# Optimization experiments

Measured on AMD Instinct MI355X. Metric: run time of the kernel, lower is better.

The kernel has to match this reference:

```python
import jax, jax.numpy as jnp
import numpy as np

D_IN = 32
D_MODEL = 128
B, T = 512, 512
INPUT_DIM = 2 * D_IN  # concat_mask=True, d_u=0


def setup_inputs() -> dict:
    key = jax.random.key(0)
    ks = jax.random.split(key, 8)
    scale = 0.05
    return {
        "x": jax.random.normal(ks[0], (B, T, D_IN), dtype=jnp.float32),
        "W_ih": jax.random.normal(ks[1], (3 * D_MODEL, INPUT_DIM), dtype=jnp.float32) * scale,
        "W_hh": jax.random.normal(ks[2], (3 * D_MODEL, D_MODEL), dtype=jnp.float32) * scale,
        "b_ih": jax.random.normal(ks[3], (3 * D_MODEL,), dtype=jnp.float32) * scale,
        "b_hh": jax.random.normal(ks[4], (3 * D_MODEL,), dtype=jnp.float32) * scale,
        "W_out": jax.random.normal(ks[5], (D_IN, D_MODEL), dtype=jnp.float32) * scale,
        "b_out": jax.random.normal(ks[6], (D_IN,), dtype=jnp.float32) * scale,
        "mask": jax.random.randint(ks[7], (B, T, D_IN), 0, 2, dtype=jnp.int32),
    }


def reference(x, W_ih, W_hh, b_ih, b_hh, W_out, b_out, mask):
    m_bool = mask.astype(bool)                      # [B,T,d_in]
    m_f = mask.astype(x.dtype)
    x = jnp.where(m_bool, x, jnp.zeros_like(x))     # zero-fill missing

    h0 = jnp.zeros((x.shape[0], D_MODEL), dtype=x.dtype)   # state_init='zero'
    x_hat0 = h0 @ W_out.T + b_out                   # readout of initial state

    def gru_cell(x_t, h):
        gx = x_t @ W_ih.T + b_ih                    # [B, 3*d_model]
        gh = h @ W_hh.T + b_hh
        xr, xz, xn = jnp.split(gx, 3, axis=-1)
        hr, hz, hn = jnp.split(gh, 3, axis=-1)
        r = jax.nn.sigmoid(xr + hr)
        z = jax.nn.sigmoid(xz + hz)
        n = jnp.tanh(xn + r * hn)
        return (1.0 - z) * n + z * h

    def step(carry, inp):
        h, x_hat = carry
        x_s, mb_s, mf_s = inp                       # [B,d_in] each
        x_p = jnp.where(mb_s, x_s, x_hat)           # fill blanks with prediction
        x_t = jnp.concatenate([x_p, mf_s], axis=-1) # concat_mask=True
        h_new = gru_cell(x_t, h)
        x_hat_new = h_new @ W_out.T + b_out
        return (h_new, x_hat_new), x_hat_new

    # scan over steps 0..T-2 (time-major)
    xs = jnp.swapaxes(x[:, :-1], 0, 1)              # [T-1, B, d_in]
    mbs = jnp.swapaxes(m_bool[:, :-1], 0, 1)
    mfs = jnp.swapaxes(m_f[:, :-1], 0, 1)
    _, preds = jax.lax.scan(step, (h0, x_hat0), (xs, mbs, mfs))  # [T-1, B, d_in]

    out = jnp.concatenate([x_hat0[None], preds], axis=0)         # [T, B, d_in]
    return jnp.swapaxes(out, 0, 1)                                # [B, T, d_in]
```

## Files before the change

### kernel.cpp

```cpp
#include <hip/hip_runtime.h>
#include <hip/hip_bf16.h>

#define D_IN 32
#define TT 512
#define GB 16
#define NBLK 32
#define MAGIC 0x51F7C0DEu

typedef __attribute__((ext_vector_type(8))) short bf16x8;
typedef __attribute__((ext_vector_type(4))) float f32x4;
typedef __attribute__((ext_vector_type(4))) int   i32x4;

__device__ inline short bf16_of(float f) {
    union { float f; unsigned u; } v; v.f = f;
    unsigned r = v.u + 0x7FFFu + ((v.u >> 16) & 1u);
    return (short)(r >> 16);
}
__device__ inline unsigned cvt_pk_bf16(float lo, float hi) {
    unsigned r;
    asm("v_cvt_pk_bf16_f32 %0, %1, %2" : "=v"(r) : "v"(lo), "v"(hi));
    return r;
}
__device__ inline bf16x8 load8_bf16(const float* __restrict__ p) {
    bf16x8 r;
#pragma unroll
    for (int e = 0; e < 8; ++e) r[e] = bf16_of(p[e]);
    return r;
}
__device__ inline bf16x8 load44_bf16(const float* __restrict__ p, int qq) {
    bf16x8 r;
#pragma unroll
    for (int e = 0; e < 4; ++e) {
        r[e]     = bf16_of(p[qq * 4 + e]);
        r[4 + e] = bf16_of(p[16 + qq * 4 + e]);
    }
    return r;
}
__device__ inline f32x4 splat4(float v) { return (f32x4){v, v, v, v}; }

__device__ inline float sigmoid_fast(float x) {
    return __builtin_amdgcn_rcpf(1.0f + __expf(-x));
}
__device__ inline float tanh_fast(float x) {
    return 1.0f - 2.0f * __builtin_amdgcn_rcpf(__expf(2.0f * x) + 1.0f);
}
__device__ inline void lds_barrier() {
    asm volatile("s_waitcnt lgkmcnt(0)\n\ts_barrier" ::: "memory");
}

#define MFMA16(A, B, C) __builtin_amdgcn_mfma_f32_16x16x32_bf16(A, B, C, 0, 0, 0)

__global__ __launch_bounds__(512, 2)
void rnn_imputer(const float* __restrict__ x,
                 const float* __restrict__ W_ih,
                 const float* __restrict__ W_hh,
                 const float* __restrict__ b_ih,
                 const float* __restrict__ b_hh,
                 const float* __restrict__ W_out,
                 const float* __restrict__ b_out,
                 const int*   __restrict__ mask,
                 float* __restrict__ out,
                 unsigned*    flags,
                 int          use_spin) {
    if (blockIdx.x >= NBLK) {
        if (!use_spin || threadIdx.x >= 64) return;
        const unsigned long long t0 = __builtin_amdgcn_s_memrealtime();
        float a0 = 1.0f + threadIdx.x * 1e-6f, a1 = a0 + 0.1f, a2 = a0 + 0.2f,
              a3 = a0 + 0.3f, a4 = a0 + 0.4f, a5 = a0 + 0.5f, a6 = a0 + 0.6f,
              a7 = a0 + 0.7f;
        for (;;) {
            unsigned acc = 0;
#pragma unroll
            for (int j = 0; j < NBLK; ++j)
                acc |= (__hip_atomic_load(&flags[j], __ATOMIC_RELAXED,
                                          __HIP_MEMORY_SCOPE_AGENT) ^ MAGIC);
            if (acc == 0) break;
            if (__builtin_amdgcn_s_memrealtime() - t0 > 200000ull) break;
            for (int i = 0; i < 32; ++i) {
                a0 = __builtin_fmaf(a0, 1.0000001f, 1e-8f);
                a1 = __builtin_fmaf(a1, 1.0000001f, 1e-8f);
                a2 = __builtin_fmaf(a2, 1.0000001f, 1e-8f);
                a3 = __builtin_fmaf(a3, 1.0000001f, 1e-8f);
                a4 = __builtin_fmaf(a4, 1.0000001f, 1e-8f);
                a5 = __builtin_fmaf(a5, 1.0000001f, 1e-8f);
                a6 = __builtin_fmaf(a6, 1.0000001f, 1e-8f);
                a7 = __builtin_fmaf(a7, 1.0000001f, 1e-8f);
            }
            __builtin_amdgcn_s_sleep(8);
        }
        const float s = a0 + a1 + a2 + a3 + a4 + a5 + a6 + a7;
        if (s == 1.2345e30f) ((float*)flags)[NBLK + 1] = s;
        return;
    }

    __shared__ __align__(16) float xch[16][GB][36];
    __shared__ __align__(16) int   mch[16][GB][36];
    __shared__ __align__(16) short hbuf[2][GB][136];

    const int tid  = threadIdx.x;
    const int wv   = tid >> 6;
    const int lane = tid & 63;
    const int q    = lane >> 4;
    const int c    = lane & 15;
    const int bb   = blockIdx.x * GB;
    const int brow = bb + c;
    const int i_col = wv * 16 + c;

    bf16x8 Br[6], Bz[6], Bxn[2], Bhn[4];
    Br[0]  = load44_bf16(W_ih + (size_t)i_col * 64, q);
    Br[1]  = load44_bf16(W_ih + (size_t)i_col * 64 + 32, q);
    Bz[0]  = load44_bf16(W_ih + (size_t)(128 + i_col) * 64, q);
    Bz[1]  = load44_bf16(W_ih + (size_t)(128 + i_col) * 64 + 32, q);
    Bxn[0] = load44_bf16(W_ih + (size_t)(256 + i_col) * 64, q);
    Bxn[1] = load44_bf16(W_ih + (size_t)(256 + i_col) * 64 + 32, q);
#pragma unroll
    for (int kt = 2; kt < 6; ++kt) {
        const int k = (kt - 2) * 32 + q * 8;
        Br[kt] = load8_bf16(W_hh + (size_t)i_col * 128 + k);
        Bz[kt] = load8_bf16(W_hh + (size_t)(128 + i_col) * 128 + k);
    }
#pragma unroll
    for (int kt = 0; kt < 4; ++kt)
        Bhn[kt] = load8_bf16(W_hh + (size_t)(256 + i_col) * 128 + kt * 32 + q * 8);

    bf16x8 Ao[2][4];
#pragma unroll
    for (int ta = 0; ta < 2; ++ta)
#pragma unroll
        for (int kt = 0; kt < 4; ++kt)
            Ao[ta][kt] = load8_bf16(W_out + (size_t)(ta * 16 + c) * 128 + kt * 32 + q * 8);

    f32x4 bo_v[2];
#pragma unroll
    for (int ta = 0; ta < 2; ++ta)
        bo_v[ta] = *(const f32x4*)&b_out[ta * 16 + q * 4];

    const float bR  = b_ih[i_col]       + b_hh[i_col];
    const float bZ  = b_ih[128 + i_col] + b_hh[128 + i_col];
    const float bXN = b_ih[256 + i_col];
    const float bHN = b_hh[256 + i_col];

    float h_reg[4] = {0.f, 0.f, 0.f, 0.f};

    bf16x8 A0, A1;
    {
        const size_t o = (size_t)brow * TT * D_IN;
        const f32x4 xa = *(const f32x4*)&x[o + q * 4];
        const f32x4 xb = *(const f32x4*)&x[o + 16 + q * 4];
        const i32x4 ma = *(const i32x4*)&mask[o + q * 4];
        const i32x4 mb = *(const i32x4*)&mask[o + 16 + q * 4];
        union { bf16x8 v; unsigned d[4]; } a0, a1;
#pragma unroll
        for (int j = 0; j < 4; ++j) {
            const float fa = ma[j] ? xa[j] : b_out[q * 4 + j];
            const float fb = mb[j] ? xb[j] : b_out[16 + q * 4 + j];
            ((short*)&a0.v)[j]     = bf16_of(fa);
            ((short*)&a0.v)[4 + j] = bf16_of(fb);
            ((short*)&a1.v)[j]     = ma[j] ? (short)0x3F80 : (short)0;
            ((short*)&a1.v)[4 + j] = mb[j] ? (short)0x3F80 : (short)0;
        }
        A0 = a0.v; A1 = a1.v;
    }
#pragma unroll
    for (int ta = 0; ta < 2; ++ta)
        if (wv == ta)
            *(f32x4*)&out[(size_t)brow * TT * D_IN + ta * 16 + q * 4] = bo_v[ta];

#pragma unroll
    for (int rnd = 0; rnd < 4; ++rnd) {
        const int ts  = 1 + rnd * 4 + (tid >> 7);
        const int row = (tid >> 3) & 15;
        const int c4  = (tid & 7) * 4;
        const size_t o = ((size_t)(bb + row) * TT + ts) * D_IN + c4;
        *(f32x4*)&xch[ts & 15][row][c4] = *(const f32x4*)&x[o];
        *(i32x4*)&mch[ts & 15][row][c4] = *(const i32x4*)&mask[o];
    }

    f32x4 Ra = splat4(0.f), Rb = splat4(0.f);
    f32x4 Za = splat4(0.f), Zb = splat4(0.f);
    f32x4 HNa = splat4(bHN), HNb = splat4(0.f);
    f32x4 Rc  = MFMA16(A1, Br[1],  splat4(bR));
    f32x4 Zc  = MFMA16(A1, Bz[1],  splat4(bZ));
    f32x4 XNc = MFMA16(A1, Bxn[1], splat4(bXN));

    f32x4 sgx[2] = {splat4(0.f), splat4(0.f)};
    i32x4 sgm[2] = {(i32x4){0,0,0,0}, (i32x4){0,0,0,0}};

    __syncthreads();

    for (int t = 0; t < TT - 1; ++t) {
        Rc  = MFMA16(A0, Br[0],  Rc);
        Zc  = MFMA16(A0, Bz[0],  Zc);
        XNc = MFMA16(A0, Bxn[0], XNc);

        const int sl = (t + 1) & 15;
        const f32x4 pfx0 = *(const f32x4*)&xch[sl][c][q * 4];
        const f32x4 pfx1 = *(const f32x4*)&xch[sl][c][16 + q * 4];
        const i32x4 pfm0 = *(const i32x4*)&mch[sl][c][q * 4];
        const i32x4 pfm1 = *(const i32x4*)&mch[sl][c][16 + q * 4];

        {
            union { bf16x8 v; unsigned d[4]; } a1;
            a1.d[0] = (pfm0[0] ? 0x3F80u : 0u) | ((pfm0[1] ? 0x3F80u : 0u) << 16);
            a1.d[1] = (pfm0[2] ? 0x3F80u : 0u) | ((pfm0[3] ? 0x3F80u : 0u) << 16);
            a1.d[2] = (pfm1[0] ? 0x3F80u : 0u) | ((pfm1[1] ? 0x3F80u : 0u) << 16);
            a1.d[3] = (pfm1[2] ? 0x3F80u : 0u) | ((pfm1[3] ? 0x3F80u : 0u) << 16);
            A1 = a1.v;
        }
        f32x4 RcN  = MFMA16(A1, Br[1],  splat4(bR));
        f32x4 ZcN  = MFMA16(A1, Bz[1],  splat4(bZ));
        f32x4 XNcN = MFMA16(A1, Bxn[1], splat4(bXN));

        if ((t & 7) == 0 && t) {
#pragma unroll
            for (int rnd = 0; rnd < 2; ++rnd) {
                const int tsu = t + 8 + rnd * 4 + (tid >> 7);
                const int row = (tid >> 3) & 15;
                const int c4  = (tid & 7) * 4;
                *(f32x4*)&xch[tsu & 15][row][c4] = sgx[rnd];
                *(i32x4*)&mch[tsu & 15][row][c4] = sgm[rnd];
            }
        }
        if ((t & 7) == 7) {
#pragma unroll
            for (int rnd = 0; rnd < 2; ++rnd) {
                const int tsu = t + 9 + rnd * 4 + (tid >> 7);
                const int ts  = tsu <= TT - 1 ? tsu : TT - 1;
                const int row = (tid >> 3) & 15;
                const int c4  = (tid & 7) * 4;
                const size_t o = ((size_t)(bb + row) * TT + ts) * D_IN + c4;
                sgx[rnd] = *(const f32x4*)&x[o];
                sgm[rnd] = *(const i32x4*)&mask[o];
            }
        }

        const int pb = (t + 1) & 1;
        float hn[4];
#pragma unroll
        for (int r = 0; r < 4; ++r) {
            const float rr = sigmoid_fast(Ra[r] + Rb[r] + Rc[r]);
            const float zz = sigmoid_fast(Za[r] + Zb[r] + Zc[r]);
            const float nn = tanh_fast(XNc[r] + rr * (HNa[r] + HNb[r]));
            const float h  = nn + zz * (h_reg[r] - nn);
            h_reg[r] = h;
            hn[r] = h;
        }
        {
            const unsigned pk0 = cvt_pk_bf16(hn[0], hn[1]);
            const unsigned pk1 = cvt_pk_bf16(hn[2], hn[3]);
            hbuf[pb][q * 4 + 0][i_col] = (short)(pk0 & 0xFFFFu);
            hbuf[pb][q * 4 + 1][i_col] = (short)(pk0 >> 16);
            hbuf[pb][q * 4 + 2][i_col] = (short)(pk1 & 0xFFFFu);
            hbuf[pb][q * 4 + 3][i_col] = (short)(pk1 >> 16);
        }

        lds_barrier();

        bf16x8 Ah[4];
#pragma unroll
        for (int kt = 0; kt < 4; ++kt)
            Ah[kt] = *(const bf16x8*)&hbuf[pb][c][kt * 32 + q * 8];

        f32x4 o00 = MFMA16(Ao[0][0], Ah[0], bo_v[0]);
        f32x4 o10 = MFMA16(Ao[1][0], Ah[0], bo_v[1]);
        f32x4 o01 = MFMA16(Ao[0][1], Ah[1], splat4(0.f));
        f32x4 o11 = MFMA16(Ao[1][1], Ah[1], splat4(0.f));
        f32x4 o02 = MFMA16(Ao[0][2], Ah[2], splat4(0.f));
        f32x4 o12 = MFMA16(Ao[1][2], Ah[2], splat4(0.f));
        f32x4 o03 = MFMA16(Ao[0][3], Ah[3], splat4(0.f));
        f32x4 o13 = MFMA16(Ao[1][3], Ah[3], splat4(0.f));

        Ra  = MFMA16(Ah[0], Br[2], splat4(0.f));
        Za  = MFMA16(Ah[0], Bz[2], splat4(0.f));
        HNa = MFMA16(Ah[0], Bhn[0], splat4(bHN));
        Rb  = MFMA16(Ah[2], Br[4], splat4(0.f));
        Zb  = MFMA16(Ah[2], Bz[4], splat4(0.f));
        HNb = MFMA16(Ah[2], Bhn[2], splat4(0.f));
        Ra  = MFMA16(Ah[1], Br[3], Ra);
        Za  = MFMA16(Ah[1], Bz[3], Za);
        HNa = MFMA16(Ah[1], Bhn[1], HNa);
        Rb  = MFMA16(Ah[3], Br[5], Rb);
        Zb  = MFMA16(Ah[3], Bz[5], Zb);
        HNb = MFMA16(Ah[3], Bhn[3], HNb);

        {
            f32x4 xh0, xh1;
#pragma unroll
            for (int r = 0; r < 4; ++r) {
                xh0[r] = (o00[r] + o01[r]) + (o02[r] + o03[r]);
                xh1[r] = (o10[r] + o11[r]) + (o12[r] + o13[r]);
            }
            if (wv == 0)
                *(f32x4*)&out[((size_t)brow * TT + (t + 1)) * D_IN + q * 4] = xh0;
            if (wv == 1)
                *(f32x4*)&out[((size_t)brow * TT + (t + 1)) * D_IN + 16 + q * 4] = xh1;

            const float v00 = pfm0[0] ? pfx0[0] : xh0[0];
            const float v01 = pfm0[1] ? pfx0[1] : xh0[1];
            const float v02 = pfm0[2] ? pfx0[2] : xh0[2];
            const float v03 = pfm0[3] ? pfx0[3] : xh0[3];
            const float v10 = pfm1[0] ? pfx1[0] : xh1[0];
            const float v11 = pfm1[1] ? pfx1[1] : xh1[1];
            const float v12 = pfm1[2] ? pfx1[2] : xh1[2];
            const float v13 = pfm1[3] ? pfx1[3] : xh1[3];
            union { bf16x8 v; unsigned d[4]; } a0;
            a0.d[0] = cvt_pk_bf16(v00, v01);
            a0.d[1] = cvt_pk_bf16(v02, v03);
            a0.d[2] = cvt_pk_bf16(v10, v11);
            a0.d[3] = cvt_pk_bf16(v12, v13);
            A0 = a0.v;
        }

        Rc = RcN; Zc = ZcN; XNc = XNcN;
    }

    if (use_spin && tid == 0)
        __hip_atomic_store(&flags[blockIdx.x], MAGIC, __ATOMIC_RELAXED,
                           __HIP_MEMORY_SCOPE_AGENT);
}

extern "C" void kernel_launch(void* const* d_in, const int* in_sizes, int n_in,
                              void* d_out, int out_size, void* d_ws, size_t ws_size,
                              hipStream_t stream) {
    const float* x     = (const float*)d_in[0];
    const float* W_ih  = (const float*)d_in[1];
    const float* W_hh  = (const float*)d_in[2];
    const float* b_ih  = (const float*)d_in[3];
    const float* b_hh  = (const float*)d_in[4];
    const float* W_out = (const float*)d_in[5];
    const float* b_out = (const float*)d_in[6];
    const int*   mask  = (const int*)d_in[7];
    float* out = (float*)d_out;

    const int use_spin = (d_ws != nullptr && ws_size >= 256) ? 1 : 0;
    const int grid = use_spin ? 256 : NBLK;

    rnn_imputer<<<dim3(grid), dim3(512), 0, stream>>>(
        x, W_ih, W_hh, b_ih, b_hh, W_out, b_out, mask, out,
        (unsigned*)d_ws, use_spin);
}
```

Baseline: 664.6 us.

## Replace LDS x/mask staging with per-thread register prefetch and re-chain gate MFMAs

Removes the shared-memory ring buffer that staged x and mask in chunks of 8 steps. Each thread now loads its own row's x/mask for step t+2 directly from global memory into registers, one step ahead. The gate MFMA accumulation chains are reorganised so the mask-half of the input projection folds into the hidden accumulators, and the readout sums are chained pairwise. It also requests 72KB of dynamic shared memory, which likely limits how many blocks share a CU (the spin blocks). The trade is one global-load latency exposed per step against less LDS traffic and no periodic staging work.

```diff
diff --git a/kernel.cpp b/kernel.cpp
--- a/kernel.cpp
+++ b/kernel.cpp
@@ -49,6 +49,8 @@
 }
 
 #define MFMA16(A, B, C) __builtin_amdgcn_mfma_f32_16x16x32_bf16(A, B, C, 0, 0, 0)
+
+extern __shared__ char dyn_pad[];
 
 __global__ __launch_bounds__(512, 2)
 void rnn_imputer(const float* __restrict__ x,
@@ -93,8 +95,6 @@
         return;
     }
 
-    __shared__ __align__(16) float xch[16][GB][36];
-    __shared__ __align__(16) int   mch[16][GB][36];
     __shared__ __align__(16) short hbuf[2][GB][136];
 
     const int tid  = threadIdx.x;
@@ -142,13 +142,15 @@
 
     float h_reg[4] = {0.f, 0.f, 0.f, 0.f};
 
+    const float* xrow = x    + (size_t)brow * TT * D_IN + q * 4;
+    const int*   mrow = mask + (size_t)brow * TT * D_IN + q * 4;
+
     bf16x8 A0, A1;
     {
-        const size_t o = (size_t)brow * TT * D_IN;
-        const f32x4 xa = *(const f32x4*)&x[o + q * 4];
-        const f32x4 xb = *(const f32x4*)&x[o + 16 + q * 4];
-        const i32x4 ma = *(const i32x4*)&mask[o + q * 4];
-        const i32x4 mb = *(const i32x4*)&mask[o + 16 + q * 4];
+        const f32x4 xa = *(const f32x4*)&xrow[0];
+        const f32x4 xb = *(const f32x4*)&xrow[16];
+        const i32x4 ma = *(const i32x4*)&mrow[0];
+        const i32x4 mb = *(const i32x4*)&mrow[16];
         union { bf16x8 v; unsigned d[4]; } a0, a1;
 #pragma unroll
         for (int j = 0; j < 4; ++j) {
@@ -166,38 +168,82 @@
         if (wv == ta)
             *(f32x4*)&out[(size_t)brow * TT * D_IN + ta * 16 + q * 4] = bo_v[ta];
 
-#pragma unroll
-    for (int rnd = 0; rnd < 4; ++rnd) {
-        const int ts  = 1 + rnd * 4 + (tid >> 7);
-        const int row = (tid >> 3) & 15;
-        const int c4  = (tid & 7) * 4;
-        const size_t o = ((size_t)(bb + row) * TT + ts) * D_IN + c4;
-        *(f32x4*)&xch[ts & 15][row][c4] = *(const f32x4*)&x[o];
-        *(i32x4*)&mch[ts & 15][row][c4] = *(const i32x4*)&mask[o];
-    }
-
-    f32x4 Ra = splat4(0.f), Rb = splat4(0.f);
-    f32x4 Za = splat4(0.f), Zb = splat4(0.f);
+    f32x4 gx0 = *(const f32x4*)&xrow[1 * D_IN];
+    f32x4 gx1 = *(const f32x4*)&xrow[1 * D_IN + 16];
+    i32x4 gm0 = *(const i32x4*)&mrow[1 * D_IN];
+    i32x4 gm1 = *(const i32x4*)&mrow[1 * D_IN + 16];
+
+    f32x4 Ra = MFMA16(A1, Br[1],  splat4(bR));
+    f32x4 Za = MFMA16(A1, Bz[1],  splat4(bZ));
+    f32x4 XNa = MFMA16(A1, Bxn[1], splat4(bXN));
+    f32x4 Rb = splat4(0.f), Zb = splat4(0.f);
     f32x4 HNa = splat4(bHN), HNb = splat4(0.f);
-    f32x4 Rc  = MFMA16(A1, Br[1],  splat4(bR));
-    f32x4 Zc  = MFMA16(A1, Bz[1],  splat4(bZ));
-    f32x4 XNc = MFMA16(A1, Bxn[1], splat4(bXN));
-
-    f32x4 sgx[2] = {splat4(0.f), splat4(0.f)};
-    i32x4 sgm[2] = {(i32x4){0,0,0,0}, (i32x4){0,0,0,0}};
-
-    __syncthreads();
 
     for (int t = 0; t < TT - 1; ++t) {
-        Rc  = MFMA16(A0, Br[0],  Rc);
-        Zc  = MFMA16(A0, Bz[0],  Zc);
-        XNc = MFMA16(A0, Bxn[0], XNc);
-
-        const int sl = (t + 1) & 15;
-        const f32x4 pfx0 = *(const f32x4*)&xch[sl][c][q * 4];
-        const f32x4 pfx1 = *(const f32x4*)&xch[sl][c][16 + q * 4];
-        const i32x4 pfm0 = *(const i32x4*)&mch[sl][c][q * 4];
-        const i32x4 pfm1 = *(const i32x4*)&mch[sl][c][16 + q * 4];
+        Rb = MFMA16(A0, Br[0],  Rb);
+        Zb = MFMA16(A0, Bz[0],  Zb);
+        const f32x4 XNb = MFMA16(A0, Bxn[0], splat4(0.f));
+
+        const f32x4 pfx0 = gx0;
+        const f32x4 pfx1 = gx1;
+        const i32x4 pfm0 = gm0;
+        const i32x4 pfm1 = gm1;
+
+        const int ts2 = (t + 2 <= TT - 1) ? (t + 2) : (TT - 1);
+        const size_t o2 = (size_t)ts2 * D_IN;
+        const f32x4 nx0 = *(const f32x4*)&xrow[o2];
+        const f32x4 nx1 = *(const f32x4*)&xrow[o2 + 16];
+        const i32x4 nm0 = *(const i32x4*)&mrow[o2];
+        const i32x4 nm1 = *(const i32x4*)&mrow[o2 + 16];
+
+        const int pb = (t + 1) & 1;
+        float hn[4];
+#pragma unroll
+        for (int r = 0; r < 4; ++r) {
+            const float rr = sigmoid_fast(Ra[r] + Rb[r]);
+            const float zz = sigmoid_fast(Za[r] + Zb[r]);
+            const float nn = tanh_fast(XNa[r] + XNb[r] + rr * (HNa[r] + HNb[r]));
+            const float h  = nn + zz * (h_reg[r] - nn);
+            h_reg[r] = h;
+            hn[r] = h;
+        }
+        {
+            const unsigned pk0 = cvt_pk_bf16(hn[0], hn[1]);
+            const unsigned pk1 = cvt_pk_bf16(hn[2], hn[3]);
+            hbuf[pb][q * 4 + 0][i_col] = (short)(pk0 & 0xFFFFu);
+            hbuf[pb][q * 4 + 1][i_col] = (short)(pk0 >> 16);
+            hbuf[pb][q * 4 + 2][i_col] = (short)(pk1 & 0xFFFFu);
+            hbuf[pb][q * 4 + 3][i_col] = (short)(pk1 >> 16);
+        }
+
+        lds_barrier();
+
+        bf16x8 Ah[4];
+#pragma unroll
+        for (int kt = 0; kt < 4; ++kt)
+            Ah[kt] = *(const bf16x8*)&hbuf[pb][c][kt * 32 + q * 8];
+
+        f32x4 aO0a = MFMA16(Ao[0][0], Ah[0], bo_v[0]);
+        f32x4 aO1a = MFMA16(Ao[1][0], Ah[0], bo_v[1]);
+        f32x4 aO0b = MFMA16(Ao[0][2], Ah[2], splat4(0.f));
+        f32x4 aO1b = MFMA16(Ao[1][2], Ah[2], splat4(0.f));
+        aO0a = MFMA16(Ao[0][1], Ah[1], aO0a);
+        aO1a = MFMA16(Ao[1][1], Ah[1], aO1a);
+        aO0b = MFMA16(Ao[0][3], Ah[3], aO0b);
+        aO1b = MFMA16(Ao[1][3], Ah[3], aO1b);
+
+        Ra  = MFMA16(Ah[0], Br[2], splat4(bR));
+        Za  = MFMA16(Ah[0], Bz[2], splat4(bZ));
+        HNa = MFMA16(Ah[0], Bhn[0], splat4(bHN));
+        Rb  = MFMA16(Ah[2], Br[4], splat4(0.f));
+        Zb  = MFMA16(Ah[2], Bz[4], splat4(0.f));
+        Ra  = MFMA16(Ah[1], Br[3], Ra);
+        Za  = MFMA16(Ah[1], Bz[3], Za);
+        HNa = MFMA16(Ah[1], Bhn[1], HNa);
+        Rb  = MFMA16(Ah[3], Br[5], Rb);
+        Zb  = MFMA16(Ah[3], Bz[5], Zb);
+        HNb = MFMA16(Ah[2], Bhn[2], splat4(0.f));
+        HNb = MFMA16(Ah[3], Bhn[3], HNb);
 
         {
             union { bf16x8 v; unsigned d[4]; } a1;
@@ -207,88 +253,16 @@
             a1.d[3] = (pfm1[2] ? 0x3F80u : 0u) | ((pfm1[3] ? 0x3F80u : 0u) << 16);
             A1 = a1.v;
         }
-        f32x4 RcN  = MFMA16(A1, Br[1],  splat4(bR));
-        f32x4 ZcN  = MFMA16(A1, Bz[1],  splat4(bZ));
-        f32x4 XNcN = MFMA16(A1, Bxn[1], splat4(bXN));
-
-        if ((t & 7) == 0 && t) {
-#pragma unroll
-            for (int rnd = 0; rnd < 2; ++rnd) {
-                const int tsu = t + 8 + rnd * 4 + (tid >> 7);
-                const int row = (tid >> 3) & 15;
-                const int c4  = (tid & 7) * 4;
-                *(f32x4*)&xch[tsu & 15][row][c4] = sgx[rnd];
-                *(i32x4*)&mch[tsu & 15][row][c4] = sgm[rnd];
-            }
-        }
-        if ((t & 7) == 7) {
-#pragma unroll
-            for (int rnd = 0; rnd < 2; ++rnd) {
-                const int tsu = t + 9 + rnd * 4 + (tid >> 7);
-                const int ts  = tsu <= TT - 1 ? tsu : TT - 1;
-                const int row = (tid >> 3) & 15;
-                const int c4  = (tid & 7) * 4;
-                const size_t o = ((size_t)(bb + row) * TT + ts) * D_IN + c4;
-                sgx[rnd] = *(const f32x4*)&x[o];
-                sgm[rnd] = *(const i32x4*)&mask[o];
-            }
-        }
-
-        const int pb = (t + 1) & 1;
-        float hn[4];
-#pragma unroll
-        for (int r = 0; r < 4; ++r) {
-            const float rr = sigmoid_fast(Ra[r] + Rb[r] + Rc[r]);
-            const float zz = sigmoid_fast(Za[r] + Zb[r] + Zc[r]);
-            const float nn = tanh_fast(XNc[r] + rr * (HNa[r] + HNb[r]));
-            const float h  = nn + zz * (h_reg[r] - nn);
-            h_reg[r] = h;
-            hn[r] = h;
-        }
-        {
-            const unsigned pk0 = cvt_pk_bf16(hn[0], hn[1]);
-            const unsigned pk1 = cvt_pk_bf16(hn[2], hn[3]);
-            hbuf[pb][q * 4 + 0][i_col] = (short)(pk0 & 0xFFFFu);
-            hbuf[pb][q * 4 + 1][i_col] = (short)(pk0 >> 16);
-            hbuf[pb][q * 4 + 2][i_col] = (short)(pk1 & 0xFFFFu);
-            hbuf[pb][q * 4 + 3][i_col] = (short)(pk1 >> 16);
-        }
-
-        lds_barrier();
-
-        bf16x8 Ah[4];
-#pragma unroll
-        for (int kt = 0; kt < 4; ++kt)
-            Ah[kt] = *(const bf16x8*)&hbuf[pb][c][kt * 32 + q * 8];
-
-        f32x4 o00 = MFMA16(Ao[0][0], Ah[0], bo_v[0]);
-        f32x4 o10 = MFMA16(Ao[1][0], Ah[0], bo_v[1]);
-        f32x4 o01 = MFMA16(Ao[0][1], Ah[1], splat4(0.f));
-        f32x4 o11 = MFMA16(Ao[1][1], Ah[1], splat4(0.f));
-        f32x4 o02 = MFMA16(Ao[0][2], Ah[2], splat4(0.f));
-        f32x4 o12 = MFMA16(Ao[1][2], Ah[2], splat4(0.f));
-        f32x4 o03 = MFMA16(Ao[0][3], Ah[3], splat4(0.f));
-        f32x4 o13 = MFMA16(Ao[1][3], Ah[3], splat4(0.f));
-
-        Ra  = MFMA16(Ah[0], Br[2], splat4(0.f));
-        Za  = MFMA16(Ah[0], Bz[2], splat4(0.f));
-        HNa = MFMA16(Ah[0], Bhn[0], splat4(bHN));
-        Rb  = MFMA16(Ah[2], Br[4], splat4(0.f));
-        Zb  = MFMA16(Ah[2], Bz[4], splat4(0.f));
-        HNb = MFMA16(Ah[2], Bhn[2], splat4(0.f));
-        Ra  = MFMA16(Ah[1], Br[3], Ra);
-        Za  = MFMA16(Ah[1], Bz[3], Za);
-        HNa = MFMA16(Ah[1], Bhn[1], HNa);
-        Rb  = MFMA16(Ah[3], Br[5], Rb);
-        Zb  = MFMA16(Ah[3], Bz[5], Zb);
-        HNb = MFMA16(Ah[3], Bhn[3], HNb);
+        Ra  = MFMA16(A1, Br[1],  Ra);
+        Za  = MFMA16(A1, Bz[1],  Za);
+        XNa = MFMA16(A1, Bxn[1], splat4(bXN));
 
         {
             f32x4 xh0, xh1;
 #pragma unroll
             for (int r = 0; r < 4; ++r) {
-                xh0[r] = (o00[r] + o01[r]) + (o02[r] + o03[r]);
-                xh1[r] = (o10[r] + o11[r]) + (o12[r] + o13[r]);
+                xh0[r] = aO0a[r] + aO0b[r];
+                xh1[r] = aO1a[r] + aO1b[r];
             }
             if (wv == 0)
                 *(f32x4*)&out[((size_t)brow * TT + (t + 1)) * D_IN + q * 4] = xh0;
@@ -311,7 +285,7 @@
             A0 = a0.v;
         }
 
-        Rc = RcN; Zc = ZcN; XNc = XNcN;
+        gx0 = nx0; gx1 = nx1; gm0 = nm0; gm1 = nm1;
     }
 
     if (use_spin && tid == 0)
@@ -335,7 +309,7 @@
     const int use_spin = (d_ws != nullptr && ws_size >= 256) ? 1 : 0;
     const int grid = use_spin ? 256 : NBLK;
 
-    rnn_imputer<<<dim3(grid), dim3(512), 0, stream>>>(
+    rnn_imputer<<<dim3(grid), dim3(512), 73728, stream>>>(
         x, W_ih, W_hh, b_ih, b_hh, W_out, b_out, mask, out,
         (unsigned*)d_ws, use_spin);
 }
```

Measured after the change: 684.6 us. 3.0% more time.
